# Kernel optimization log

Measured on AMD Instinct MI355X. Metric: run time of the kernel, lower is better.

The kernel has to match this reference:

```python
import jax, jax.numpy as jnp
import numpy as np

EPS = 1e-06
K = 10
N, M, D, C = 65536, 1024, 2, 3


def setup_inputs() -> dict:
    key = jax.random.key(0)
    k1, k2, k3, k4 = jax.random.split(key, 4)
    x = jax.random.uniform(k1, (N, D), dtype=jnp.float32)            # query points (pixels)
    mus = jax.random.uniform(k2, (1, M, D), dtype=jnp.float32)        # gaussian means
    A = 0.1 * jax.random.normal(k3, (1, M, D, D), dtype=jnp.float32)  # random factor
    covs = A @ jnp.swapaxes(A, -1, -2) + 0.01 * jnp.eye(D, dtype=jnp.float32)  # SPD covariances
    cols = jax.random.uniform(k4, (1, M, C), dtype=jnp.float32)       # per-gaussian RGB
    return {"x": x, "mus": mus, "covs": covs, "cols": cols}


def reference(x, mus, covs, cols):
    # d: [N, M, D] point-to-mean offsets
    d = x[:, None, :] - mus[0]
    # solve covs @ s = d for each (point, gaussian) pair -> [N, M, D]
    s = jnp.linalg.solve(covs[0], d[..., None])[..., 0]
    # quadratic form d^T Sigma^{-1} d -> gaussian weights [N, M]
    gauss = jnp.exp(-0.5 * jnp.einsum('nmd,nmd->nm', d, s))
    k = min(K, mus.shape[1])
    vals, idx = jax.lax.top_k(gauss, k)              # [N, k]
    top_cols = cols[0][idx]                           # [N, k, C]
    raw = jnp.einsum('nk,nkc->nc', vals, top_cols)    # weighted color sum
    return raw / (vals.sum(-1, keepdims=True) + EPS)  # normalized [N, C]
```

## Files before the change

kernel.cpp:

```cpp
#include <hip/hip_runtime.h>
#include <stdint.h>

#define MG 1024
#define KTOP 10
#define EPSF 1e-6f
#define CXc 48
#define CYc 32
#define NCELL (CXc * CYc)
#define SCX 96
#define SCY 32
#define NSUB (SCX * SCY)
#define CAPS 64
#define OVCAP 256
#define RHO 0.01878f
#define CSTRIDE 1040
#define MAXC 500
#define LPAD 512
#define CPAD 16
#define POISON 0xAAAAAAAAu

typedef unsigned long long u64;
typedef unsigned short u16;

__global__ __launch_bounds__(256) void k_prep(
    const float* __restrict__ x, const float* __restrict__ mus,
    const float* __restrict__ covs,
    uint32_t* __restrict__ counts, uint32_t* __restrict__ ovc,
    u16* __restrict__ ovlist, u16* __restrict__ buckets,
    float4* __restrict__ grec, float* __restrict__ grecC,
    u16* __restrict__ candM, uint32_t* __restrict__ ncand, int N)
{
    const int t = threadIdx.x, blk = blockIdx.x;
    if (blk < 256) {
        const int n = blk * 256 + t;
        if (n < MG) {
            const float4 cv = ((const float4*)covs)[n];
            const float2 mu = ((const float2*)mus)[n];
            const float inv = 1.0f / (cv.x * cv.w - cv.y * cv.z);
            grec[n]  = make_float4(mu.x, mu.y, -0.5f * cv.w * inv, cv.y * inv);
            grecC[n] = -0.5f * cv.x * inv;
        }
        if (n >= N) return;
        const float2 xv = ((const float2*)x)[n];
        int six = (int)(xv.x * SCX); six = six < 0 ? 0 : (six > SCX - 1 ? SCX - 1 : six);
        int siy = (int)(xv.y * SCY); siy = siy < 0 ? 0 : (siy > SCY - 1 ? SCY - 1 : siy);
        const int sub = siy * SCX + six;
        const uint32_t r = atomicAdd(&counts[sub * CPAD], 1u) - POISON;
        if (r < CAPS) buckets[sub * CAPS + r] = (u16)n;
        else { const uint32_t o = atomicAdd(ovc, 1u) - POISON; if (o < OVCAP) ovlist[o] = (u16)n; }
        return;
    }
    const int lane = t & 63;
    const int c = (blk - 256) * 4 + (t >> 6);
    const float cx = ((float)(c % CXc) + 0.5f) / (float)CXc;
    const float cy = ((float)(c / CXc) + 0.5f) / (float)CYc;
    const float INF = __builtin_huge_valf();

    float D10[KTOP], Uv[16], Dv[16];
    #pragma unroll
    for (int i = 0; i < KTOP; ++i) D10[i] = -INF;

    #pragma unroll
    for (int j = 0; j < 16; ++j) {
        const int m = j * 64 + lane;
        const float4 cv = ((const float4*)covs)[m];
        const float2 mu = ((const float2*)mus)[m];
        const float inv = 1.0f / (cv.x * cv.w - cv.y * cv.z);
        const float A = -0.5f * cv.w * inv, B = cv.y * inv, Cc = -0.5f * cv.x * inv;
        const float dx = cx - mu.x, dy = cy - mu.y;
        const float qc = fmaf(fmaf(A, dx, B * dy), dx, Cc * (dy * dy));
        const float S00 = -2.0f * A, S01 = -B, S11 = -2.0f * Cc;
        const float sx = S00 * dx + S01 * dy, sy = S01 * dx + S11 * dy;
        const float slack = sqrtf(fmaf(sx, sx, sy * sy)) * RHO;
        const float lr2 = 0.5f * (S00 + S11) * (RHO * RHO);
        const float eps = 1e-3f * (1.0f + fabsf(qc) + slack);
        Uv[j] = qc + slack + eps;
        const float D = qc - slack - lr2 - eps;
        Dv[j] = D;
        bool cg[KTOP];
        #pragma unroll
        for (int i = 0; i < KTOP; ++i) cg[i] = D10[i] >= D;
        #pragma unroll
        for (int i = KTOP - 1; i >= 1; --i)
            D10[i] = cg[i] ? D10[i] : (cg[i - 1] ? D : D10[i - 1]);
        D10[0] = cg[0] ? D10[0] : D;
    }
    #pragma unroll
    for (int s = 1; s < 64; s <<= 1) {
        float ob[KTOP], na[KTOP];
        #pragma unroll
        for (int i = 0; i < KTOP; ++i) ob[i] = __shfl_xor(D10[i], s);
        #pragma unroll
        for (int i = 0; i < KTOP; ++i) {
            float best = -INF;
            #pragma unroll
            for (int j = 0; j <= i + 1 && j <= KTOP; ++j) {
                const int l = i + 1 - j;
                if (l > KTOP) continue;
                const float av = (j == 0) ? INF : D10[j - 1];
                const float bv = (l == 0) ? INF : ob[l - 1];
                best = fmaxf(best, fminf(av, bv));
            }
            na[i] = best;
        }
        #pragma unroll
        for (int i = 0; i < KTOP; ++i) D10[i] = na[i];
    }
    const float L = D10[KTOP - 1];

    const int base = c * CSTRIDE;
    const u64 below = (lane == 0) ? 0ull : ((~0ull) >> (64 - lane));
    int total = 0;
    #pragma unroll
    for (int j = 0; j < 16; ++j) {
        const bool keep = (Dv[j] >= L);
        const u64 bal = __ballot(keep);
        if (keep) candM[base + total + (int)__popcll(bal & below)] = (u16)(j * 64 + lane);
        total += (int)__popcll(bal);
    }
    #pragma unroll
    for (int j = 0; j < 16; ++j) {
        const bool keep = (Uv[j] >= L) && (Dv[j] < L);
        const u64 bal = __ballot(keep);
        if (keep) candM[base + total + (int)__popcll(bal & below)] = (u16)(j * 64 + lane);
        total += (int)__popcll(bal);
    }
    if (lane == 0) ncand[c] = (uint32_t)total;
}

__global__ __launch_bounds__(128) void k_main(
    const float* __restrict__ x, const float* __restrict__ cols,
    const float4* __restrict__ grec, const float* __restrict__ grecC,
    const uint32_t* __restrict__ counts, const uint32_t* __restrict__ ovc,
    const u16* __restrict__ ovlist, const u16* __restrict__ buckets,
    const u16* __restrict__ candM, const uint32_t* __restrict__ ncand,
    float* __restrict__ out, int N)
{
    __shared__ float4 l4[LPAD];
    __shared__ __align__(16) float lC[LPAD];
    __shared__ __align__(16) uint32_t lM[LPAD];

    const int t = threadIdx.x;
    const int lane = t & 63, wv = t >> 6;
    const int b = blockIdx.x;

    u64 topk[KTOP];
    const u64 SENT = ((u64)0x007FFFFFull) << 10;
    #pragma unroll
    for (int j = 0; j < KTOP; ++j) topk[j] = SENT;
    float thr = __uint_as_float(0xff800000u);

    auto net_insert = [&](u64 key) {
        bool cg[KTOP];
        #pragma unroll
        for (int j = 0; j < KTOP; ++j) cg[j] = topk[j] >= key;
        #pragma unroll
        for (int j = KTOP - 1; j >= 1; --j)
            topk[j] = cg[j] ? topk[j] : (cg[j - 1] ? key : topk[j - 1]);
        topk[0] = cg[0] ? topk[0] : key;
    };
    auto ins = [&](float q, int m) {
        if (__any(q >= thr)) {
            const uint32_t bb = __float_as_uint(q);
            const uint32_t msk = (uint32_t)((int32_t)bb >> 31) | 0x80000000u;
            net_insert(((u64)(bb ^ msk) << 10) | (u64)(MG - 1 - m));
            const uint32_t kb = (uint32_t)(topk[KTOP - 1] >> 10);
            const uint32_t db = ((int32_t)kb < 0) ? (kb ^ 0x80000000u) : ~kb;
            thr = __uint_as_float(db);
        }
    };
    auto full_scan = [&](float x0, float x1) {
        for (int m = 0; m < MG; m += 4) {
            const float4 g0 = grec[m], g1 = grec[m + 1], g2 = grec[m + 2], g3 = grec[m + 3];
            const float4 c4 = *(const float4*)&grecC[m];
            const float dx0 = x0 - g0.x, dy0 = x1 - g0.y;
            const float dx1 = x0 - g1.x, dy1 = x1 - g1.y;
            const float dx2 = x0 - g2.x, dy2 = x1 - g2.y;
            const float dx3 = x0 - g3.x, dy3 = x1 - g3.y;
            const float q0 = fmaf(fmaf(g0.z, dx0, g0.w * dy0), dx0, c4.x * (dy0 * dy0));
            const float q1 = fmaf(fmaf(g1.z, dx1, g1.w * dy1), dx1, c4.y * (dy1 * dy1));
            const float q2 = fmaf(fmaf(g2.z, dx2, g2.w * dy2), dx2, c4.z * (dy2 * dy2));
            const float q3 = fmaf(fmaf(g3.z, dx3, g3.w * dy3), dx3, c4.w * (dy3 * dy3));
            const float qm = fmaxf(fmaxf(q0, q1), fmaxf(q2, q3));
            if (__any(qm >= thr)) {
                ins(q0, m); ins(q1, m + 1); ins(q2, m + 2); ins(q3, m + 3);
            }
        }
    };

    int pp = 0; bool valid = false;

    if (b >= NCELL) {
        const uint32_t oc = min(ovc[0] - POISON, (uint32_t)OVCAP);
        const uint32_t gi = (uint32_t)((b - NCELL) * 128 + t);
        if (__ballot(gi < oc) == 0ull) return;
        int p = -1;
        if (gi < oc) p = (int)ovlist[gi];
        valid = (p >= 0);
        const int p0lane = __shfl(p, 0);
        pp = valid ? p : (p0lane >= 0 ? p0lane : 0);
        const float2 xv = ((const float2*)x)[pp];
        full_scan(xv.x, xv.y);
    } else {
        const int c = b;
        const int ccx = c % CXc, ccy = c / CXc;
        const int sub0 = ccy * SCX + 2 * ccx;
        const int cnt0 = (int)min(counts[sub0 * CPAD] - POISON, (uint32_t)CAPS);
        const int cnt1 = (int)min(counts[(sub0 + 1) * CPAD] - POISON, (uint32_t)CAPS);
        const int cnt = cnt0 + cnt1;
        if (cnt == 0) return;

        const int nc = (int)min(ncand[c], (uint32_t)(CSTRIDE - 8));
        const bool staged = (nc <= MAXC);
        int ntot = 0;
        if (staged) {
            ntot = (nc + 7) & ~7;
            const int cbase = c * CSTRIDE;
            for (int i = t; i < ntot; i += 128) {
                if (i < nc) {
                    const int m = (int)candM[cbase + i];
                    l4[i] = grec[m];
                    lC[i] = grecC[m];
                    lM[i] = (uint32_t)m;
                } else {
                    l4[i] = make_float4(3e30f, 3e30f, -1.0f, 0.0f);
                    lC[i] = -1.0f;
                    lM[i] = 0u;
                }
            }
            __syncthreads();
        }

        const int slot = wv * 64 + lane;
        if (wv * 64 >= cnt) return;
        int p = -1;
        if (slot < cnt) {
            p = (slot < cnt0) ? (int)buckets[sub0 * CAPS + slot]
                              : (int)buckets[(sub0 + 1) * CAPS + (slot - cnt0)];
        }
        valid = (p >= 0);
        const int p0lane = __shfl(p, 0);
        pp = valid ? p : p0lane;
        const float2 xv = ((const float2*)x)[pp];
        const float x0 = xv.x, x1 = xv.y;

        if (staged) {
            for (int i2 = 0; i2 < ntot; i2 += 8) {
                const float4 g0 = l4[i2],   g1 = l4[i2+1], g2 = l4[i2+2], g3 = l4[i2+3];
                const float4 g4 = l4[i2+4], g5 = l4[i2+5], g6 = l4[i2+6], g7 = l4[i2+7];
                const float4 ca = *(const float4*)&lC[i2];
                const float4 cb = *(const float4*)&lC[i2 + 4];
                const float dx0 = x0-g0.x, dy0 = x1-g0.y;
                const float dx1 = x0-g1.x, dy1 = x1-g1.y;
                const float dx2 = x0-g2.x, dy2 = x1-g2.y;
                const float dx3 = x0-g3.x, dy3 = x1-g3.y;
                const float dx4 = x0-g4.x, dy4 = x1-g4.y;
                const float dx5 = x0-g5.x, dy5 = x1-g5.y;
                const float dx6 = x0-g6.x, dy6 = x1-g6.y;
                const float dx7 = x0-g7.x, dy7 = x1-g7.y;
                const float q0 = fmaf(fmaf(g0.z, dx0, g0.w*dy0), dx0, ca.x*(dy0*dy0));
                const float q1 = fmaf(fmaf(g1.z, dx1, g1.w*dy1), dx1, ca.y*(dy1*dy1));
                const float q2 = fmaf(fmaf(g2.z, dx2, g2.w*dy2), dx2, ca.z*(dy2*dy2));
                const float q3 = fmaf(fmaf(g3.z, dx3, g3.w*dy3), dx3, ca.w*(dy3*dy3));
                const float q4 = fmaf(fmaf(g4.z, dx4, g4.w*dy4), dx4, cb.x*(dy4*dy4));
                const float q5 = fmaf(fmaf(g5.z, dx5, g5.w*dy5), dx5, cb.y*(dy5*dy5));
                const float q6 = fmaf(fmaf(g6.z, dx6, g6.w*dy6), dx6, cb.z*(dy6*dy6));
                const float q7 = fmaf(fmaf(g7.z, dx7, g7.w*dy7), dx7, cb.w*(dy7*dy7));
                const float qm = fmaxf(fmaxf(fmaxf(q0,q1), fmaxf(q2,q3)),
                                       fmaxf(fmaxf(q4,q5), fmaxf(q6,q7)));
                if (__any(qm >= thr)) {
                    const uint4 ma = *(const uint4*)&lM[i2];
                    const uint4 mb = *(const uint4*)&lM[i2 + 4];
                    ins(q0, (int)ma.x); ins(q1, (int)ma.y);
                    ins(q2, (int)ma.z); ins(q3, (int)ma.w);
                    ins(q4, (int)mb.x); ins(q5, (int)mb.y);
                    ins(q6, (int)mb.z); ins(q7, (int)mb.w);
                }
            }
        } else {
            full_scan(x0, x1);
        }
    }

    float vsum = 0.0f, rc = 0.0f, gc = 0.0f, bc = 0.0f;
    #pragma unroll
    for (int j = 0; j < KTOP; ++j) {
        const u64 key = topk[j];
        const int m = (MG - 1) - (int)(key & 1023u);
        const uint32_t kb = (uint32_t)(key >> 10);
        const uint32_t bb = ((int32_t)kb < 0) ? (kb ^ 0x80000000u) : ~kb;
        const float v = __expf(__uint_as_float(bb));
        vsum += v;
        rc = fmaf(v, cols[3 * m + 0], rc);
        gc = fmaf(v, cols[3 * m + 1], gc);
        bc = fmaf(v, cols[3 * m + 2], bc);
    }
    const float s = 1.0f / (vsum + EPSF);
    if (valid) {
        out[pp * 3 + 0] = rc * s;
        out[pp * 3 + 1] = gc * s;
        out[pp * 3 + 2] = bc * s;
    }
}

extern "C" void kernel_launch(void* const* d_in, const int* in_sizes, int n_in,
                              void* d_out, int out_size, void* d_ws, size_t ws_size,
                              hipStream_t stream) {
    const float* x    = (const float*)d_in[0];
    const float* mus  = (const float*)d_in[1];
    const float* covs = (const float*)d_in[2];
    const float* cols = (const float*)d_in[3];
    float* out = (float*)d_out;
    const int N = in_sizes[0] / 2;

    uint32_t* counts = (uint32_t*)d_ws;
    uint32_t* ovc    = counts + NSUB * CPAD;
    u16*      ovlist = (u16*)(ovc + 16);
    uintptr_t a = (uintptr_t)(ovlist + OVCAP);
    a = (a + 15) & ~(uintptr_t)15;
    float4*   grec   = (float4*)a;
    float*    grecC  = (float*)(grec + MG);
    u16*      buckets= (u16*)(grecC + MG);
    uint32_t* ncand  = (uint32_t*)(buckets + NSUB * CAPS);
    u16*      candM  = (u16*)(ncand + NCELL);
    const size_t need = ((char*)(candM + NCELL * CSTRIDE)) - (char*)d_ws;

    if (ws_size >= need) {
        k_prep<<<256 + NCELL / 4, 256, 0, stream>>>(x, mus, covs, counts, ovc,
                                                    ovlist, buckets, grec, grecC,
                                                    candM, ncand, N);
        k_main<<<NCELL + 2, 128, 0, stream>>>(x, cols, grec, grecC,
                                              counts, ovc, ovlist, buckets,
                                              candM, ncand, out, N);
    }
}
```

Baseline: 82.43 us.

## Sort cell candidates into bound bins and early-exit batches below top-k threshold

The prep kernel now groups each cell's candidate gaussians into bins by how their upper bound compares with the cell's top-10 lower bounds. It also writes a per-8-candidate batch bound array. The main kernel loads that bound before each batch of 8 and stops scanning once no lane's current threshold can be beaten. This cuts the number of quadratic-form evaluations per pixel, at the cost of extra ballot passes in prep, a global load per batch and a wave-wide vote in the inner loop.

```diff
diff --git a/kernel.cpp b/kernel.cpp
--- a/kernel.cpp
+++ b/kernel.cpp
@@ -14,6 +14,7 @@
 #define OVCAP 256
 #define RHO 0.01878f
 #define CSTRIDE 1040
+#define NBATCH 132
 #define MAXC 500
 #define LPAD 512
 #define CPAD 16
@@ -28,7 +29,8 @@
     uint32_t* __restrict__ counts, uint32_t* __restrict__ ovc,
     u16* __restrict__ ovlist, u16* __restrict__ buckets,
     float4* __restrict__ grec, float* __restrict__ grecC,
-    u16* __restrict__ candM, uint32_t* __restrict__ ncand, int N)
+    u16* __restrict__ candM, float* __restrict__ candB,
+    uint32_t* __restrict__ ncand, int N)
 {
     const int t = threadIdx.x, blk = blockIdx.x;
     if (blk < 256) {
@@ -56,7 +58,7 @@
     const float cy = ((float)(c / CXc) + 0.5f) / (float)CYc;
     const float INF = __builtin_huge_valf();
 
-    float D10[KTOP], Uv[16], Dv[16];
+    float D10[KTOP], Uv[16];
     #pragma unroll
     for (int i = 0; i < KTOP; ++i) D10[i] = -INF;
 
@@ -76,7 +78,6 @@
         const float eps = 1e-3f * (1.0f + fabsf(qc) + slack);
         Uv[j] = qc + slack + eps;
         const float D = qc - slack - lr2 - eps;
-        Dv[j] = D;
         bool cg[KTOP];
         #pragma unroll
         for (int i = 0; i < KTOP; ++i) cg[i] = D10[i] >= D;
@@ -108,22 +109,40 @@
     }
     const float L = D10[KTOP - 1];
 
+    int binv[16];
+    #pragma unroll
+    for (int j = 0; j < 16; ++j) {
+        int bin = 0;
+        #pragma unroll
+        for (int i = 0; i < KTOP; ++i) bin += (Uv[j] < D10[i]) ? 1 : 0;
+        binv[j] = (Uv[j] >= L) ? bin : 99;
+    }
     const int base = c * CSTRIDE;
     const u64 below = (lane == 0) ? 0ull : ((~0ull) >> (64 - lane));
     int total = 0;
-    #pragma unroll
-    for (int j = 0; j < 16; ++j) {
-        const bool keep = (Dv[j] >= L);
-        const u64 bal = __ballot(keep);
-        if (keep) candM[base + total + (int)__popcll(bal & below)] = (u16)(j * 64 + lane);
-        total += (int)__popcll(bal);
-    }
-    #pragma unroll
-    for (int j = 0; j < 16; ++j) {
-        const bool keep = (Uv[j] >= L) && (Dv[j] < L);
-        const u64 bal = __ballot(keep);
-        if (keep) candM[base + total + (int)__popcll(bal & below)] = (u16)(j * 64 + lane);
-        total += (int)__popcll(bal);
+    int binStart[KTOP];
+    #pragma unroll
+    for (int bb = 0; bb < KTOP; ++bb) {
+        binStart[bb] = total;
+        #pragma unroll
+        for (int j = 0; j < 16; ++j) {
+            const bool inb = (binv[j] == bb);
+            const u64 bal = __ballot(inb);
+            if (inb) candM[base + total + (int)__popcll(bal & below)] = (u16)(j * 64 + lane);
+            total += (int)__popcll(bal);
+        }
+    }
+    for (int ib = lane; ib < NBATCH; ib += 64) {
+        const int s = 8 * ib;
+        float bnd;
+        if (s >= total) bnd = -INF;
+        else {
+            int bb = 0;
+            #pragma unroll
+            for (int k = 1; k < KTOP; ++k) bb += (s >= binStart[k]) ? 1 : 0;
+            bnd = (bb == 0) ? INF : D10[bb - 1];
+        }
+        candB[c * NBATCH + ib] = bnd;
     }
     if (lane == 0) ncand[c] = (uint32_t)total;
 }
@@ -133,8 +152,8 @@
     const float4* __restrict__ grec, const float* __restrict__ grecC,
     const uint32_t* __restrict__ counts, const uint32_t* __restrict__ ovc,
     const u16* __restrict__ ovlist, const u16* __restrict__ buckets,
-    const u16* __restrict__ candM, const uint32_t* __restrict__ ncand,
-    float* __restrict__ out, int N)
+    const u16* __restrict__ candM, const float* __restrict__ candB,
+    const uint32_t* __restrict__ ncand, float* __restrict__ out, int N)
 {
     __shared__ float4 l4[LPAD];
     __shared__ __align__(16) float lC[LPAD];
@@ -245,7 +264,10 @@
         const float x0 = xv.x, x1 = xv.y;
 
         if (staged) {
+            const int cb8 = c * NBATCH;
             for (int i2 = 0; i2 < ntot; i2 += 8) {
+                const float bnd = candB[cb8 + (i2 >> 3)];
+                if (!__any(bnd >= thr)) break;
                 const float4 g0 = l4[i2],   g1 = l4[i2+1], g2 = l4[i2+2], g3 = l4[i2+3];
                 const float4 g4 = l4[i2+4], g5 = l4[i2+5], g6 = l4[i2+6], g7 = l4[i2+7];
                 const float4 ca = *(const float4*)&lC[i2];
@@ -323,14 +345,17 @@
     u16*      buckets= (u16*)(grecC + MG);
     uint32_t* ncand  = (uint32_t*)(buckets + NSUB * CAPS);
     u16*      candM  = (u16*)(ncand + NCELL);
-    const size_t need = ((char*)(candM + NCELL * CSTRIDE)) - (char*)d_ws;
+    uintptr_t a2 = (uintptr_t)(candM + NCELL * CSTRIDE);
+    a2 = (a2 + 15) & ~(uintptr_t)15;
+    float*    candB  = (float*)a2;
+    const size_t need = ((char*)(candB + NCELL * NBATCH)) - (char*)d_ws;
 
     if (ws_size >= need) {
         k_prep<<<256 + NCELL / 4, 256, 0, stream>>>(x, mus, covs, counts, ovc,
                                                     ovlist, buckets, grec, grecC,
-                                                    candM, ncand, N);
+                                                    candM, candB, ncand, N);
         k_main<<<NCELL + 2, 128, 0, stream>>>(x, cols, grec, grecC,
                                               counts, ovc, ovlist, buckets,
-                                              candM, ncand, out, N);
+                                              candM, candB, ncand, out, N);
     }
 }
```

New measurement: 88.05 us. 6.8% more time.
